# Performance work log

Hardware: AMD Instinct MI355X
Metric: run time of the kernel (lower is better)

## Reference

```python
import jax, jax.numpy as jnp
import numpy as np
from jax import lax


def _mdlstm_dir(x, Wx, Wh, Wv, b):
    # x: [H, W, B, Cin]; one diagonal-causal 2D-LSTM scan (top-left origin).
    H, W, B, Cin = x.shape
    C = Wh.shape[0]
    xa = jnp.einsum('hwbi,ic->hwbc', x, Wx) + b  # [H,W,B,5C] precomputed input gates

    def col_step(carry, inp):
        h_l, c_l = carry                    # left neighbor [B,C]
        xa_ij, h_u, c_u = inp               # input preact, up neighbor
        a = xa_ij + h_l @ Wh + h_u @ Wv     # [B,5C]
        i, f1, f2, o, g = jnp.split(a, 5, axis=-1)
        c = jax.nn.sigmoid(i) * jnp.tanh(g) + jax.nn.sigmoid(f1) * c_l + jax.nn.sigmoid(f2) * c_u
        h = jax.nn.sigmoid(o) * jnp.tanh(c)
        return (h, c), (h, c)

    z = jnp.zeros((B, C), x.dtype)
    zrow = jnp.zeros((W, B, C), x.dtype)

    def row_step(carry, xa_row):
        h_up, c_up = carry                  # [W,B,C]
        _, (hs, cs) = lax.scan(col_step, (z, z), (xa_row, h_up, c_up))
        return (hs, cs), hs

    _, hh = lax.scan(row_step, (zrow, zrow), xa)  # [H,W,B,C]
    return hh


def _mdlstm4(x, Wx, Wh, Wv, b):
    # x: [B,Cin,H,W] -> per-direction outputs [4,H,W,B,C] (directions: TL, TR, BL, BR origins)
    xt = jnp.transpose(x, (2, 3, 0, 1))  # [H,W,B,Cin]
    x4 = jnp.stack([xt, xt[:, ::-1], xt[::-1], xt[::-1, ::-1]])
    o = jax.vmap(_mdlstm_dir)(x4, Wx, Wh, Wv, b)  # [4,H,W,B,C]
    return jnp.stack([o[0], o[1][:, ::-1], o[2][::-1], o[3][::-1, ::-1]])


def _block(x, Wx, Wh, Wv, b, cw, cb):
    h4 = _mdlstm4(x, Wx, Wh, Wv, b)            # [4,H,W,B,C]
    h = jnp.transpose(h4.sum(0), (2, 3, 0, 1))  # sum directions -> [B,C,H,W]
    y = lax.conv_general_dilated(h, cw, window_strides=(2, 2), padding='VALID',
                                 dimension_numbers=('NCHW', 'OIHW', 'NCHW'))
    return jnp.tanh(y + cb[None, :, None, None])


def _forward(x, p0_Wx, p0_Wh, p0_Wv, p0_b, c0_w, c0_b,
             p1_Wx, p1_Wh, p1_Wv, p1_b, c1_w, c1_b,
             p2_Wx, p2_Wh, p2_Wv, p2_b, dW, db):
    x = _block(x, p0_Wx, p0_Wh, p0_Wv, p0_b, c0_w, c0_b)  # [B,6,31,126]
    x = _block(x, p1_Wx, p1_Wh, p1_Wv, p1_b, c1_w, c1_b)  # [B,20,14,61]
    h4 = _mdlstm4(x, p2_Wx, p2_Wh, p2_Wv, p2_b)           # [4,H,W,B,50]
    # per-direction Linear(50->100) then sum over the 4 directions
    out = jnp.einsum('dhwbc,dcn->bhwn', h4, dW) + db.sum(0)
    return out  # [B,14,61,100]


def setup_inputs() -> dict:
    key = jax.random.key(0)
    ks = jax.random.split(key, 20)
    rn = lambda k, s, sc=0.1: jax.random.normal(k, s, jnp.float32) * sc
    return {
        'x': jax.random.normal(ks[0], (16, 1, 64, 256), jnp.float32),
        'p0_Wx': rn(ks[1], (4, 1, 10)), 'p0_Wh': rn(ks[2], (4, 2, 10)),
        'p0_Wv': rn(ks[3], (4, 2, 10)), 'p0_b': rn(ks[4], (4, 10)),
        'c0_w': rn(ks[5], (6, 2, 2, 4)), 'c0_b': rn(ks[6], (6,)),
        'p1_Wx': rn(ks[7], (4, 6, 50)), 'p1_Wh': rn(ks[8], (4, 10, 50)),
        'p1_Wv': rn(ks[9], (4, 10, 50)), 'p1_b': rn(ks[10], (4, 50)),
        'c1_w': rn(ks[11], (20, 10, 2, 4)), 'c1_b': rn(ks[12], (20,)),
        'p2_Wx': rn(ks[13], (4, 20, 250)), 'p2_Wh': rn(ks[14], (4, 50, 250)),
        'p2_Wv': rn(ks[15], (4, 50, 250)), 'p2_b': rn(ks[16], (4, 250)),
        'dW': rn(ks[17], (4, 50, 100)), 'db': rn(ks[18], (4, 100)),
    }


def reference(x, p0_Wx, p0_Wh, p0_Wv, p0_b, c0_w, c0_b,
              p1_Wx, p1_Wh, p1_Wv, p1_b, c1_w, c1_b,
              p2_Wx, p2_Wh, p2_Wv, p2_b, dW, db):
    return _forward(x, p0_Wx, p0_Wh, p0_Wv, p0_b, c0_w, c0_b,
                    p1_Wx, p1_Wh, p1_Wv, p1_b, c1_w, c1_b,
                    p2_Wx, p2_Wh, p2_Wv, p2_b, dW, db)
```

## Files before the change

kernel.cpp:

```cpp
#include <hip/hip_runtime.h>

typedef unsigned short ushort_t;
typedef __attribute__((ext_vector_type(8))) short short8;
typedef __attribute__((ext_vector_type(4))) float float4_t;
typedef __attribute__((ext_vector_type(2))) float v2f;

__device__ __forceinline__ float frcp(float x) { return __builtin_amdgcn_rcpf(x); }
__device__ __forceinline__ float fsig(float x) { return frcp(1.f + __expf(-x)); }
__device__ __forceinline__ float ftanh(float x) { return 1.f - 2.f * frcp(1.f + __expf(2.f * x)); }
__device__ __forceinline__ float sig_e2(float a) { return frcp(1.f + __builtin_amdgcn_exp2f(a)); }
__device__ __forceinline__ float th_e2(float a) { return 1.f - 2.f * frcp(1.f + __builtin_amdgcn_exp2f(a)); }

__device__ __forceinline__ ushort_t f2bf(float f) {
    union { float f; unsigned u; } v; v.f = f;
    unsigned u = v.u;
    unsigned r = (u + 0x7fffu + ((u >> 16) & 1u)) >> 16;
    return (ushort_t)r;
}
__device__ __forceinline__ float bf2f(ushort_t s) {
    union { unsigned u; float f; } v; v.u = ((unsigned)s) << 16;
    return v.f;
}
__device__ __forceinline__ float dpp_shr1(float x) {
    int i = __builtin_bit_cast(int, x);
    int r = __builtin_amdgcn_update_dpp(0, i, 0x138 , 0xf, 0xf, true);
    return __builtin_bit_cast(float, r);
}

__global__ __launch_bounds__(64) void k_mdlstm0(
    const float* __restrict__ x, const float* __restrict__ Wx,
    const float* __restrict__ Wh, const float* __restrict__ Wv,
    const float* __restrict__ bias, float* __restrict__ h0)
{
    const int dir = blockIdx.x >> 4, b = blockIdx.x & 15;
    const int lane = threadIdx.x;
    const bool fH = dir >= 2, fW = (dir & 1) != 0;
    const int ri = fH ? 63 - lane : lane;
    const float L2E = 1.44269504088896340736f;

    __shared__ float Xs[64 * 256];
    {
        const float* xg = x + b * 64 * 256;
        for (int i4 = lane; i4 < 4096; i4 += 64) {
            int row = i4 >> 6, c4 = (i4 & 63) << 2;
            float4 v = *(const float4*)(xg + (row << 8) + c4);
            *(float4*)&Xs[(row << 8) + c4] = v;
        }
    }
    __syncthreads();

    v2f wx[5], bs[5], wh0[5], wh1[5], wv0[5], wv1[5];
#pragma unroll
    for (int g = 0; g < 5; g++) {
        float sc = (g == 4) ? 2.f * L2E : -L2E;
#pragma unroll
        for (int un = 0; un < 2; un++) {
            int n = g * 2 + un;
            wx[g][un]  = Wx[dir * 10 + n] * sc;
            bs[g][un]  = bias[dir * 10 + n] * sc;
            wh0[g][un] = Wh[(dir * 2 + 0) * 10 + n] * sc;
            wh1[g][un] = Wh[(dir * 2 + 1) * 10 + n] * sc;
            wv0[g][un] = Wv[(dir * 2 + 0) * 10 + n] * sc;
            wv1[g][un] = Wv[(dir * 2 + 1) * 10 + n] * sc;
        }
    }

    float* orow = h0 + (((dir * 16 + b) * 64 + ri) * 256) * 2;
    v2f hr = {0.f, 0.f}, cr = {0.f, 0.f};

    auto ld = [&](int d) -> float {
        int j = d - lane; j = j < 0 ? 0 : (j > 255 ? 255 : j);
        int cj = fW ? 255 - j : j;
        return Xs[(ri << 8) + cj];
    };
    float xp0 = ld(0), xp1 = ld(1);

    for (int d = 0; d < 319; d++) {
        float xv = xp0;
        xp0 = xp1;
        xp1 = ld(d + 2);

        float hu0 = dpp_shr1(hr.x), hu1 = dpp_shr1(hr.y);
        float cu0 = dpp_shr1(cr.x), cu1 = dpp_shr1(cr.y);

        int j = d - lane;
        if (j >= 0 && j < 256) {
            v2f a[5];
#pragma unroll
            for (int g = 0; g < 5; g++) {
                v2f t = __builtin_elementwise_fma((v2f){xv, xv}, wx[g], bs[g]);
                t = __builtin_elementwise_fma((v2f){hr.x, hr.x}, wh0[g], t);
                t = __builtin_elementwise_fma((v2f){hr.y, hr.y}, wh1[g], t);
                t = __builtin_elementwise_fma((v2f){hu0, hu0}, wv0[g], t);
                t = __builtin_elementwise_fma((v2f){hu1, hu1}, wv1[g], t);
                a[g] = t;
            }
            v2f si  = {sig_e2(a[0].x), sig_e2(a[0].y)};
            v2f sf1 = {sig_e2(a[1].x), sig_e2(a[1].y)};
            v2f sf2 = {sig_e2(a[2].x), sig_e2(a[2].y)};
            v2f so  = {sig_e2(a[3].x), sig_e2(a[3].y)};
            v2f tg  = {th_e2(a[4].x),  th_e2(a[4].y)};
            v2f cu  = {cu0, cu1};
            v2f cn = si * tg + sf1 * cr + sf2 * cu;
            v2f tc = {th_e2(cn.x * (2.f * L2E)), th_e2(cn.y * (2.f * L2E))};
            hr = so * tc;
            cr = cn;
            int cj = fW ? 255 - j : j;
            float2 hv; hv.x = hr.x; hv.y = hr.y;
            *(float2*)&orow[cj * 2] = hv;
        } else {
            hr = (v2f){0.f, 0.f};
            cr = (v2f){0.f, 0.f};
        }
    }
}

__global__ __launch_bounds__(128) void k_conv0(
    const float* __restrict__ h0, const float* __restrict__ cw,
    const float* __restrict__ cb, float* __restrict__ x1)
{
    int blk = blockIdx.x;
    int oh = blk / 127, ow = blk % 127;
    int t = threadIdx.x;
    if (t >= 96) return;
    int b = t / 6, co = t % 6;
    float w[2][2][4];
#pragma unroll
    for (int ci = 0; ci < 2; ci++)
#pragma unroll
        for (int kh = 0; kh < 2; kh++)
#pragma unroll
            for (int kw = 0; kw < 4; kw++)
                w[ci][kh][kw] = cw[((co * 2 + ci) * 2 + kh) * 4 + kw];
    float acc = cb[co];
    for (int dirb = 0; dirb < 4; dirb++) {
#pragma unroll
        for (int kh = 0; kh < 2; kh++) {
#pragma unroll
            for (int kw = 0; kw < 4; kw++) {
                const float* ptr = h0 + ((((dirb * 16 + b) * 64) + (2 * oh + kh)) * 256 + (2 * ow + kw)) * 2;
                float2 hv = *(const float2*)ptr;
                acc = fmaf(hv.x, w[0][kh][kw], acc);
                acc = fmaf(hv.y, w[1][kh][kw], acc);
            }
        }
    }
    x1[((oh * 127 + ow) * 16 + b) * 6 + co] = ftanh(acc);
}

__global__ __launch_bounds__(1024, 1) void k_mdlstm1(
    const float* __restrict__ x1, const float* __restrict__ Wx,
    const float* __restrict__ Wh, const float* __restrict__ Wv,
    const float* __restrict__ bias, float* __restrict__ h1)
{
    const int dir = blockIdx.x >> 4, b = blockIdx.x & 15;
    const bool fH = dir >= 2, fW = (dir & 1) != 0;
    const int tid = threadIdx.x;
    const int wave = tid >> 6, lane = tid & 63;

    __shared__ float Xs1[32 * 127 * 6];
    __shared__ __align__(16) ushort_t Ah[2][32][40];
    __shared__ __align__(16) ushort_t Al[2][32][40];
    __shared__ float P[32][68];
    __shared__ float cbuf[2][33][12];

    for (int i = tid; i < 2 * 32 * 40; i += 1024) { ((ushort_t*)Ah)[i] = 0; ((ushort_t*)Al)[i] = 0; }
    for (int i = tid; i < 2 * 33 * 12; i += 1024) ((float*)cbuf)[i] = 0.f;
    for (int i = tid; i < 32 * 127 * 6; i += 1024)
        Xs1[i] = x1[(i / 6) * 96 + b * 6 + (i % 6)];
    __syncthreads();
    if (tid < 6) {
        int rr = fH ? 31 : 0, cc = fW ? 126 : 0;
        float xv = Xs1[(rr * 127 + cc) * 6 + tid];
        ushort_t xh = f2bf(xv);
        Ah[0][0][20 + tid] = xh;
        Al[0][0][20 + tid] = f2bf(xv - bf2f(xh));
    }

    const int mt = wave & 1, nt = wave >> 1;
    short8 bh = {0,0,0,0,0,0,0,0}, bl = {0,0,0,0,0,0,0,0};
    if (wave < 8) {
        int n = nt * 16 + (lane & 15);
#pragma unroll
        for (int jj = 0; jj < 8; jj++) {
            int k = (lane >> 4) * 8 + jj;
            float v = 0.f;
            if (n < 50) {
                if (k < 10)      v = Wh[(dir * 10 + k) * 50 + n];
                else if (k < 20) v = Wv[(dir * 10 + (k - 10)) * 50 + n];
                else if (k < 26) v = Wx[(dir * 6 + (k - 20)) * 50 + n];
            }
            ushort_t hi = f2bf(v);
            bh[jj] = (short)hi;
            bl[jj] = (short)f2bf(v - bf2f(hi));
        }
    }

    const int cell = tid / 10, u = tid % 10;
    float br[5];
#pragma unroll
    for (int g = 0; g < 5; g++) br[g] = (tid < 320) ? bias[dir * 50 + g * 10 + u] : 0.f;
    const int ri = fH ? 31 - cell : cell;
    float creg = 0.f;
    __syncthreads();

    int p = 0;
    for (int d = 0; d < 158; d++) {
        if (wave < 8) {
            const int arow = mt * 16 + (lane & 15);
            const int koff = (lane >> 4) * 8;
            short8 ah = *(const short8*)&Ah[p][arow][koff];
            short8 al = *(const short8*)&Al[p][arow][koff];
            float4_t acc = {0.f, 0.f, 0.f, 0.f};
            acc = __builtin_amdgcn_mfma_f32_16x16x32_bf16(ah, bh, acc, 0, 0, 0);
            acc = __builtin_amdgcn_mfma_f32_16x16x32_bf16(al, bh, acc, 0, 0, 0);
            acc = __builtin_amdgcn_mfma_f32_16x16x32_bf16(ah, bl, acc, 0, 0, 0);
            int col = nt * 16 + (lane & 15);
            int r0 = (lane >> 4) * 4;
#pragma unroll
            for (int r = 0; r < 4; r++) P[mt * 16 + r0 + r][col] = acc[r];
        } else if (tid >= 512 && tid < 704) {
            int s = tid - 512, xc = s / 6, ci = s % 6;
            int jn = d + 1 - xc;
            if (jn >= 0 && jn < 127) {
                int rr = fH ? 31 - xc : xc, cc = fW ? 126 - jn : jn;
                float xv = Xs1[(rr * 127 + cc) * 6 + ci];
                ushort_t xh = f2bf(xv);
                Ah[1 - p][xc][20 + ci] = xh;
                Al[1 - p][xc][20 + ci] = f2bf(xv - bf2f(xh));
            }
        }
        __syncthreads();

        if (tid < 320) {
            int j = d - cell;
            if (j >= 0 && j < 127) {
                float ai  = P[cell][u]      + br[0];
                float af1 = P[cell][10 + u] + br[1];
                float af2 = P[cell][20 + u] + br[2];
                float ao  = P[cell][30 + u] + br[3];
                float ag  = P[cell][40 + u] + br[4];
                float cu = cbuf[p][cell][u];
                float cn = fsig(ai) * ftanh(ag) + fsig(af1) * creg + fsig(af2) * cu;
                float hn = fsig(ao) * ftanh(cn);
                creg = cn;
                cbuf[1 - p][cell + 1][u] = cn;
                ushort_t hh = f2bf(hn);
                float hhf = bf2f(hh);
                ushort_t hlo = f2bf(hn - hhf);
                Ah[1 - p][cell][u] = hh;
                Al[1 - p][cell][u] = hlo;
                if (cell < 31) { Ah[1 - p][cell + 1][10 + u] = hh; Al[1 - p][cell + 1][10 + u] = hlo; }
                int cj = fW ? 126 - j : j;
                h1[(((dir * 16 + b) * 32 + ri) * 127 + cj) * 10 + u] = hn;
            }
        }
        __syncthreads();
        p ^= 1;
    }
}

__global__ __launch_bounds__(320, 1) void k_conv1(
    const float* __restrict__ h1, const float* __restrict__ cw,
    const float* __restrict__ cb, float* __restrict__ x2)
{
    int blk = blockIdx.x;
    int oh = blk / 62, ow = blk % 62;
    int t = threadIdx.x;
    int b = t / 20, co = t % 20;
    float w[10][2][4];
#pragma unroll
    for (int ci = 0; ci < 10; ci++)
#pragma unroll
        for (int kh = 0; kh < 2; kh++)
#pragma unroll
            for (int kw = 0; kw < 4; kw++)
                w[ci][kh][kw] = cw[((co * 10 + ci) * 2 + kh) * 4 + kw];
    float acc = cb[co];
    for (int dirb = 0; dirb < 4; dirb++) {
#pragma unroll
        for (int kh = 0; kh < 2; kh++) {
#pragma unroll
            for (int kw = 0; kw < 4; kw++) {
                const float* ptr = h1 + ((((dirb * 16 + b) * 32) + (2 * oh + kh)) * 127 + (2 * ow + kw)) * 10;
#pragma unroll
                for (int ci = 0; ci < 10; ci++)
                    acc = fmaf(ptr[ci], w[ci][kh][kw], acc);
            }
        }
    }
    x2[((oh * 62 + ow) * 16 + b) * 20 + co] = ftanh(acc);
}

__global__ __launch_bounds__(256) void k_prepB2(
    const float* __restrict__ Wh, const float* __restrict__ Wv,
    const float* __restrict__ Wx, ushort_t* __restrict__ Bh,
    ushort_t* __restrict__ Bl)
{
    int idx = blockIdx.x * 256 + threadIdx.x;
    if (idx >= 131072) return;
    int dir = idx >> 15; int k = (idx >> 8) & 127; int n = idx & 255;
    float v = 0.f;
    if (n < 250) {
        if (k < 50)       v = Wh[(dir * 50 + k) * 250 + n];
        else if (k < 100) v = Wv[(dir * 50 + (k - 50)) * 250 + n];
        else if (k < 120) v = Wx[(dir * 20 + (k - 100)) * 250 + n];
    }
    ushort_t hi = f2bf(v);
    Bh[idx] = hi;
    Bl[idx] = f2bf(v - bf2f(hi));
}

__global__ __launch_bounds__(1024, 1) void k_mdlstm2(
    const float* __restrict__ x2, const ushort_t* __restrict__ BmH,
    const ushort_t* __restrict__ BmL,
    const float* __restrict__ bias, float* __restrict__ h2)
{
    const int dir = blockIdx.x >> 4, b = blockIdx.x & 15;
    const bool fH = dir >= 2, fW = (dir & 1) != 0;
    const int tid = threadIdx.x;
    const int wave = tid >> 6, lane = tid & 63;

    __shared__ float Xs2[16 * 62 * 20];
    __shared__ __align__(16) ushort_t Ah[2][16][136];
    __shared__ __align__(16) ushort_t Al[2][16][136];
    __shared__ float P[16][260];
    __shared__ float cbuf[2][16][52];

    for (int i = tid; i < 2 * 16 * 136; i += 1024) { ((ushort_t*)Ah)[i] = 0; ((ushort_t*)Al)[i] = 0; }
    for (int i = tid; i < 16 * 62 * 20; i += 1024)
        Xs2[i] = x2[(i / 20) * 320 + b * 20 + (i % 20)];
    __syncthreads();
    if (tid < 20) {
        int ci = tid;
        int rr = fH ? 15 : 0, cc = fW ? 61 : 0;
        float xv = Xs2[(rr * 62 + cc) * 20 + ci];
        ushort_t xh = f2bf(xv);
        Ah[0][0][100 + ci] = xh;
        Al[0][0][100 + ci] = f2bf(xv - bf2f(xh));
    }

    short8 bfragH[4], bfragL[4];
    {
        const int n = wave * 16 + (lane & 15);
#pragma unroll
        for (int q = 0; q < 4; q++) {
#pragma unroll
            for (int jj = 0; jj < 8; jj++) {
                int k = q * 32 + (lane >> 4) * 8 + jj;
                bfragH[q][jj] = (short)BmH[(dir * 128 + k) * 256 + n];
                bfragL[q][jj] = (short)BmL[(dir * 128 + k) * 256 + n];
            }
        }
    }

    const int cell = tid / 50, u = tid % 50;
    float bi = 0, bf1 = 0, bf2v = 0, bo = 0, bg = 0;
    if (tid < 800) {
        bi   = bias[dir * 250 + u];
        bf1  = bias[dir * 250 + 50 + u];
        bf2v = bias[dir * 250 + 100 + u];
        bo   = bias[dir * 250 + 150 + u];
        bg   = bias[dir * 250 + 200 + u];
    }
    const int rr_c = fH ? 15 - cell : cell;
    float creg = 0.f;
    __syncthreads();

    int p = 0;
    for (int d = 0; d < 77; d++) {
        {
            const int arow = lane & 15;
            const int koff = (lane >> 4) * 8;
            short8 ah[4], al[4];
#pragma unroll
            for (int q = 0; q < 4; q++) {
                ah[q] = *(const short8*)&Ah[p][arow][q * 32 + koff];
                al[q] = *(const short8*)&Al[p][arow][q * 32 + koff];
            }
            float4_t acc = {0.f, 0.f, 0.f, 0.f};
#pragma unroll
            for (int q = 0; q < 4; q++) acc = __builtin_amdgcn_mfma_f32_16x16x32_bf16(ah[q], bfragH[q], acc, 0, 0, 0);
#pragma unroll
            for (int q = 0; q < 4; q++) acc = __builtin_amdgcn_mfma_f32_16x16x32_bf16(al[q], bfragH[q], acc, 0, 0, 0);
#pragma unroll
            for (int q = 0; q < 4; q++) acc = __builtin_amdgcn_mfma_f32_16x16x32_bf16(ah[q], bfragL[q], acc, 0, 0, 0);
            int col = wave * 16 + (lane & 15);
            int r0 = (lane >> 4) * 4;
#pragma unroll
            for (int r = 0; r < 4; r++) P[r0 + r][col] = acc[r];
        }
        __syncthreads();

        if (tid < 800) {
            int j = d - cell;
            if (j >= 0 && j < 62) {
                float ai  = P[cell][u] + bi;
                float af1 = P[cell][50 + u] + bf1;
                float af2 = P[cell][100 + u] + bf2v;
                float ao  = P[cell][150 + u] + bo;
                float ag  = P[cell][200 + u] + bg;
                float cu = (cell == 0) ? 0.f : cbuf[p][cell - 1][u];
                float cn = fsig(ai) * ftanh(ag) + fsig(af1) * creg + fsig(af2) * cu;
                float hn = fsig(ao) * ftanh(cn);
                creg = cn;
                cbuf[1 - p][cell][u] = cn;
                ushort_t hh = f2bf(hn);
                float hhf = bf2f(hh);
                ushort_t hlo = f2bf(hn - hhf);
                Ah[1 - p][cell][u] = hh;
                Al[1 - p][cell][u] = hlo;
                if (cell < 15) { Ah[1 - p][cell + 1][50 + u] = hh; Al[1 - p][cell + 1][50 + u] = hlo; }
                int cc = fW ? 61 - j : j;
                h2[(((dir * 16 + b) * 16 + rr_c) * 62 + cc) * 50 + u] = hn;
            }
        } else if (tid >= 832 && tid < 992) {
            int s = tid - 832;
#pragma unroll
            for (int it = 0; it < 2; it++) {
                int item = s + it * 160;
                int xc = item / 20, ci = item % 20;
                int jn = d + 1 - xc;
                if (jn >= 0 && jn < 62) {
                    int rr = fH ? 15 - xc : xc, cc = fW ? 61 - jn : jn;
                    float xv = Xs2[(rr * 62 + cc) * 20 + ci];
                    ushort_t xh = f2bf(xv);
                    Ah[1 - p][xc][100 + ci] = xh;
                    Al[1 - p][xc][100 + ci] = f2bf(xv - bf2f(xh));
                }
            }
        }
        __syncthreads();
        p ^= 1;
    }
}

__global__ __launch_bounds__(256) void k_final(
    const float* __restrict__ h2, const float* __restrict__ dW,
    const float* __restrict__ db, float* __restrict__ out)
{
    int blk = blockIdx.x;
    int r = blk / 62, c = blk % 62;
    int t = threadIdx.x;
    __shared__ float hb[3200];
    for (int i = t; i < 3200; i += 256) {
        int dirb = i / 800, rem = i % 800, b = rem / 50, u = rem % 50;
        hb[i] = h2[(((dirb * 16 + b) * 16 + r) * 62 + c) * 50 + u];
    }
    __syncthreads();
    for (int o = t; o < 1600; o += 256) {
        int b = o / 100, n = o % 100;
        float acc = db[n] + db[100 + n] + db[200 + n] + db[300 + n];
#pragma unroll
        for (int dirb = 0; dirb < 4; dirb++) {
            const float* hp = hb + (dirb * 16 + b) * 50;
            const float* wp = dW + dirb * 5000 + n;
#pragma unroll 10
            for (int cc2 = 0; cc2 < 50; cc2++)
                acc = fmaf(hp[cc2], wp[cc2 * 100], acc);
        }
        out[((b * 16 + r) * 62 + c) * 100 + n] = acc;
    }
}

extern "C" void kernel_launch(void* const* d_in, const int* in_sizes, int n_in,
                              void* d_out, int out_size, void* d_ws, size_t ws_size,
                              hipStream_t stream)
{
    const float* x     = (const float*)d_in[0];
    const float* p0_Wx = (const float*)d_in[1];
    const float* p0_Wh = (const float*)d_in[2];
    const float* p0_Wv = (const float*)d_in[3];
    const float* p0_b  = (const float*)d_in[4];
    const float* c0_w  = (const float*)d_in[5];
    const float* c0_b  = (const float*)d_in[6];
    const float* p1_Wx = (const float*)d_in[7];
    const float* p1_Wh = (const float*)d_in[8];
    const float* p1_Wv = (const float*)d_in[9];
    const float* p1_b  = (const float*)d_in[10];
    const float* c1_w  = (const float*)d_in[11];
    const float* c1_b  = (const float*)d_in[12];
    const float* p2_Wx = (const float*)d_in[13];
    const float* p2_Wh = (const float*)d_in[14];
    const float* p2_Wv = (const float*)d_in[15];
    const float* p2_b  = (const float*)d_in[16];
    const float* dW    = (const float*)d_in[17];
    const float* db    = (const float*)d_in[18];
    float* out = (float*)d_out;
    float* ws  = (float*)d_ws;

    float* h0 = ws;
    float* x1 = h0 + 2097152;
    float* h1 = x1 + 390144;
    float* x2 = h1 + 2600960;
    float* h2 = x2 + 317440;
    ushort_t* BmH = (ushort_t*)(h2 + 3174400);
    ushort_t* BmL = BmH + 131072;

    k_prepB2<<<512, 256, 0, stream>>>(p2_Wh, p2_Wv, p2_Wx, BmH, BmL);
    k_mdlstm0<<<64, 64, 0, stream>>>(x, p0_Wx, p0_Wh, p0_Wv, p0_b, h0);
    k_conv0<<<32 * 127, 128, 0, stream>>>(h0, c0_w, c0_b, x1);
    k_mdlstm1<<<64, 1024, 0, stream>>>(x1, p1_Wx, p1_Wh, p1_Wv, p1_b, h1);
    k_conv1<<<16 * 62, 320, 0, stream>>>(h1, c1_w, c1_b, x2);
    k_mdlstm2<<<64, 1024, 0, stream>>>(x2, BmH, BmL, p2_b, h2);
    k_final<<<16 * 62, 256, 0, stream>>>(h2, dW, db, out);
}
```

Measured before the change: 478.7 us.

## Split layer-0 MDLSTM hidden units across two wavefronts with LDS exchange

The layer-0 2D-LSTM kernel now runs two wavefronts per block, and each computes one of the two hidden units instead of one wavefront computing both. The other unit's hidden state is exchanged through a double-buffered shared-memory array, with a block barrier on every diagonal step. This halves the per-lane gate arithmetic on the serial critical path. In exchange it adds an LDS write, an LDS read and a __syncthreads on each of the 319 steps, which may cost as much as the arithmetic it saves.

```diff
diff --git a/kernel.cpp b/kernel.cpp
--- a/kernel.cpp
+++ b/kernel.cpp
@@ -27,46 +27,47 @@
     return __builtin_bit_cast(float, r);
 }
 
-__global__ __launch_bounds__(64) void k_mdlstm0(
+__global__ __launch_bounds__(128) void k_mdlstm0(
     const float* __restrict__ x, const float* __restrict__ Wx,
     const float* __restrict__ Wh, const float* __restrict__ Wv,
     const float* __restrict__ bias, float* __restrict__ h0)
 {
     const int dir = blockIdx.x >> 4, b = blockIdx.x & 15;
-    const int lane = threadIdx.x;
+    const int tid = threadIdx.x;
+    const int u = tid >> 6;
+    const int lane = tid & 63;
     const bool fH = dir >= 2, fW = (dir & 1) != 0;
     const int ri = fH ? 63 - lane : lane;
     const float L2E = 1.44269504088896340736f;
 
     __shared__ float Xs[64 * 256];
+    __shared__ float hbuf[2][2][64];
     {
         const float* xg = x + b * 64 * 256;
-        for (int i4 = lane; i4 < 4096; i4 += 64) {
+        for (int i4 = tid; i4 < 4096; i4 += 128) {
             int row = i4 >> 6, c4 = (i4 & 63) << 2;
             float4 v = *(const float4*)(xg + (row << 8) + c4);
             *(float4*)&Xs[(row << 8) + c4] = v;
         }
+        for (int i = tid; i < 256; i += 128) ((float*)hbuf)[i] = 0.f;
     }
     __syncthreads();
 
-    v2f wx[5], bs[5], wh0[5], wh1[5], wv0[5], wv1[5];
+    float wx[5], bs[5], whS[5], whO[5], wvS[5], wvO[5];
 #pragma unroll
     for (int g = 0; g < 5; g++) {
         float sc = (g == 4) ? 2.f * L2E : -L2E;
-#pragma unroll
-        for (int un = 0; un < 2; un++) {
-            int n = g * 2 + un;
-            wx[g][un]  = Wx[dir * 10 + n] * sc;
-            bs[g][un]  = bias[dir * 10 + n] * sc;
-            wh0[g][un] = Wh[(dir * 2 + 0) * 10 + n] * sc;
-            wh1[g][un] = Wh[(dir * 2 + 1) * 10 + n] * sc;
-            wv0[g][un] = Wv[(dir * 2 + 0) * 10 + n] * sc;
-            wv1[g][un] = Wv[(dir * 2 + 1) * 10 + n] * sc;
-        }
-    }
-
-    float* orow = h0 + (((dir * 16 + b) * 64 + ri) * 256) * 2;
-    v2f hr = {0.f, 0.f}, cr = {0.f, 0.f};
+        int n = g * 2 + u;
+        wx[g]  = Wx[dir * 10 + n] * sc;
+        bs[g]  = bias[dir * 10 + n] * sc;
+        whS[g] = Wh[(dir * 2 + u) * 10 + n] * sc;
+        whO[g] = Wh[(dir * 2 + (1 - u)) * 10 + n] * sc;
+        wvS[g] = Wv[(dir * 2 + u) * 10 + n] * sc;
+        wvO[g] = Wv[(dir * 2 + (1 - u)) * 10 + n] * sc;
+    }
+
+    float* orow = h0 + (((dir * 16 + b) * 64 + ri) * 256) * 2 + u;
+    float hr = 0.f, cr = 0.f;
 
     auto ld = [&](int d) -> float {
         int j = d - lane; j = j < 0 ? 0 : (j > 255 ? 255 : j);
@@ -75,43 +76,47 @@
     };
     float xp0 = ld(0), xp1 = ld(1);
 
+    int p = 0;
     for (int d = 0; d < 319; d++) {
         float xv = xp0;
         xp0 = xp1;
         xp1 = ld(d + 2);
 
-        float hu0 = dpp_shr1(hr.x), hu1 = dpp_shr1(hr.y);
-        float cu0 = dpp_shr1(cr.x), cu1 = dpp_shr1(cr.y);
+        float ho  = hbuf[p][1 - u][lane];
+        float hus = dpp_shr1(hr);
+        float cu  = dpp_shr1(cr);
+        float huo = dpp_shr1(ho);
 
         int j = d - lane;
         if (j >= 0 && j < 256) {
-            v2f a[5];
+            float a[5];
 #pragma unroll
             for (int g = 0; g < 5; g++) {
-                v2f t = __builtin_elementwise_fma((v2f){xv, xv}, wx[g], bs[g]);
-                t = __builtin_elementwise_fma((v2f){hr.x, hr.x}, wh0[g], t);
-                t = __builtin_elementwise_fma((v2f){hr.y, hr.y}, wh1[g], t);
-                t = __builtin_elementwise_fma((v2f){hu0, hu0}, wv0[g], t);
-                t = __builtin_elementwise_fma((v2f){hu1, hu1}, wv1[g], t);
+                float t = fmaf(xv, wx[g], bs[g]);
+                t = fmaf(hr,  whS[g], t);
+                t = fmaf(ho,  whO[g], t);
+                t = fmaf(hus, wvS[g], t);
+                t = fmaf(huo, wvO[g], t);
                 a[g] = t;
             }
-            v2f si  = {sig_e2(a[0].x), sig_e2(a[0].y)};
-            v2f sf1 = {sig_e2(a[1].x), sig_e2(a[1].y)};
-            v2f sf2 = {sig_e2(a[2].x), sig_e2(a[2].y)};
-            v2f so  = {sig_e2(a[3].x), sig_e2(a[3].y)};
-            v2f tg  = {th_e2(a[4].x),  th_e2(a[4].y)};
-            v2f cu  = {cu0, cu1};
-            v2f cn = si * tg + sf1 * cr + sf2 * cu;
-            v2f tc = {th_e2(cn.x * (2.f * L2E)), th_e2(cn.y * (2.f * L2E))};
+            float si  = sig_e2(a[0]);
+            float sf1 = sig_e2(a[1]);
+            float sf2 = sig_e2(a[2]);
+            float so  = sig_e2(a[3]);
+            float tg  = th_e2(a[4]);
+            float cn = si * tg + sf1 * cr + sf2 * cu;
+            float tc = th_e2(cn * (2.f * L2E));
             hr = so * tc;
             cr = cn;
             int cj = fW ? 255 - j : j;
-            float2 hv; hv.x = hr.x; hv.y = hr.y;
-            *(float2*)&orow[cj * 2] = hv;
+            orow[cj * 2] = hr;
         } else {
-            hr = (v2f){0.f, 0.f};
-            cr = (v2f){0.f, 0.f};
-        }
+            hr = 0.f;
+            cr = 0.f;
+        }
+        hbuf[1 - p][u][lane] = hr;
+        __syncthreads();
+        p ^= 1;
     }
 }
 
@@ -498,7 +503,7 @@
     ushort_t* BmL = BmH + 131072;
 
     k_prepB2<<<512, 256, 0, stream>>>(p2_Wh, p2_Wv, p2_Wx, BmH, BmL);
-    k_mdlstm0<<<64, 64, 0, stream>>>(x, p0_Wx, p0_Wh, p0_Wv, p0_b, h0);
+    k_mdlstm0<<<64, 128, 0, stream>>>(x, p0_Wx, p0_Wh, p0_Wv, p0_b, h0);
     k_conv0<<<32 * 127, 128, 0, stream>>>(h0, c0_w, c0_b, x1);
     k_mdlstm1<<<64, 1024, 0, stream>>>(x1, p1_Wx, p1_Wh, p1_Wv, p1_b, h1);
     k_conv1<<<16 * 62, 320, 0, stream>>>(h1, c1_w, c1_b, x2);
```

Result: no change. 470.6 us (-1.7%).
